# Kernel tuning notes

Hardware: AMD Instinct MI355X
Metric: run time of the kernel (lower is better)

## Reference

```python
import jax, jax.numpy as jnp
import numpy as np

N_NODES = 50000
N_EDGES = 800000
D_FEAT = 64
EDGE_DIM = 64


def setup_inputs() -> dict:
    key = jax.random.key(0)
    k1, k2, k3, k4 = jax.random.split(key, 4)
    node_feats = jax.random.normal(k1, (N_NODES, D_FEAT), dtype=jnp.float32)
    senders = jax.random.randint(k2, (N_EDGES,), 0, N_NODES, dtype=jnp.int32)
    receivers = jax.random.randint(k3, (N_EDGES,), 0, N_NODES, dtype=jnp.int32)
    # Dense(edge_dim) applied to concat([recv, send]) of width 2*D_FEAT
    W = jax.random.normal(k4, (2 * D_FEAT, EDGE_DIM), dtype=jnp.float32) / np.sqrt(2.0 * D_FEAT)
    b = jnp.zeros((EDGE_DIM,), dtype=jnp.float32)
    return {"node_feats": node_feats, "senders": senders, "receivers": receivers, "W": W, "b": b}


def reference(node_feats, senders, receivers, W, b):
    # gather node features at each edge endpoint: [E, D]
    feats_send = node_feats[senders]
    feats_recv = node_feats[receivers]
    # concat(recv, send) -> [E, 2D], Dense + tanh -> [E, edge_dim]
    edge_feats = jnp.concatenate([feats_recv, feats_send], axis=-1)
    return jnp.tanh(edge_feats @ W + b)
```

## Files before the change

kernel.cpp:

```cpp
#include <hip/hip_runtime.h>

#define N_EDGES 800000
#define N_NODES 50000
#define D 64

typedef __attribute__((ext_vector_type(8))) short bf16x8;
typedef __attribute__((ext_vector_type(4))) float f32x4;

#if __has_builtin(__builtin_amdgcn_exp2f)
#define EXP2F(x) __builtin_amdgcn_exp2f(x)
#else
#define EXP2F(x) __expf(0.69314718055994531f * (x))
#endif

__device__ __forceinline__ unsigned short f2bf(float f) {
    unsigned int u = __float_as_uint(f);
    u += 0x7fffu + ((u >> 16) & 1u);
    return (unsigned short)(u >> 16);
}
__device__ __forceinline__ unsigned int pack2(float a, float b) {
    return (unsigned int)f2bf(a) | ((unsigned int)f2bf(b) << 16);
}

__global__ __launch_bounds__(256) void prep(
    const float* __restrict__ nf, const float* __restrict__ W,
    unsigned short* __restrict__ nodes_bf, unsigned short* __restrict__ wfrag)
{
    if (blockIdx.x == gridDim.x - 1) {
#pragma unroll
        for (int i = 0; i < 4; ++i) {
            const int idx = i * 256 + threadIdx.x;
            const int ki = idx >> 8;
            const int nt = (idx >> 6) & 3;
            const int l  = idx & 63;
            const int m  = l & 15, q = l >> 4;
            const int kbase = ki * 32 + q * 8;
            const int n = nt * 16 + m;
            unsigned short* dst = wfrag + idx * 8;
#pragma unroll
            for (int j = 0; j < 8; ++j)
                dst[j] = f2bf(W[(kbase + j) * D + n]);
        }
    } else {
        const long base = ((long)blockIdx.x * 256 + threadIdx.x) * 8;
        if (base < (long)N_NODES * D) {
            const float4 lo = *(const float4*)(nf + base);
            const float4 hi = *(const float4*)(nf + base + 4);
            uint4 p;
            p.x = pack2(lo.x, lo.y);
            p.y = pack2(lo.z, lo.w);
            p.z = pack2(hi.x, hi.y);
            p.w = pack2(hi.z, hi.w);
            *(uint4*)(nodes_bf + base) = p;
        }
    }
}

__global__ __launch_bounds__(256) void edge_mlp(
    const unsigned short* __restrict__ nodes_bf,
    const bf16x8*        __restrict__ wfrag,
    const int*   __restrict__ senders,
    const int*   __restrict__ receivers,
    const float* __restrict__ bias,
    float*       __restrict__ out)
{
    __shared__ bf16x8 lds_b[1024];

#pragma unroll
    for (int i = 0; i < 4; ++i) {
        const int idx = i * 256 + threadIdx.x;
        lds_b[idx] = wfrag[idx];
    }
    __syncthreads();

    const int lane = threadIdx.x & 63;
    const int m    = lane & 15;
    const int q    = lane >> 4;
    const long wid = (long)blockIdx.x * 4 + (threadIdx.x >> 6);
    const long e0  = wid * 64;

    const int rv = receivers[e0 + lane];
    const int sv = senders[e0 + lane];
    int nidx[2][4];
#pragma unroll
    for (int mt = 0; mt < 4; ++mt) {
        nidx[0][mt] = __shfl(rv, mt * 16 + m, 64);
        nidx[1][mt] = __shfl(sv, mt * 16 + m, 64);
    }

    f32x4 acc[4][4];
#pragma unroll
    for (int mt = 0; mt < 4; ++mt)
#pragma unroll
        for (int nt = 0; nt < 4; ++nt)
            acc[mt][nt] = (f32x4)0.0f;

#pragma unroll
    for (int ki = 0; ki < 4; ++ki) {
        const int k0 = ki * 32 + q * 8;

        bf16x8 bfrag[4];
#pragma unroll
        for (int nt = 0; nt < 4; ++nt)
            bfrag[nt] = lds_b[(ki * 4 + nt) * 64 + lane];

        bf16x8 afrag[4];
#pragma unroll
        for (int mt = 0; mt < 4; ++mt) {
            const int node = nidx[ki >> 1][mt];
            afrag[mt] = *(const bf16x8*)(nodes_bf + node * D + (k0 & 63));
        }

#pragma unroll
        for (int mt = 0; mt < 4; ++mt)
#pragma unroll
            for (int nt = 0; nt < 4; ++nt)
                acc[mt][nt] = __builtin_amdgcn_mfma_f32_16x16x32_bf16(
                    bfrag[nt], afrag[mt], acc[mt][nt], 0, 0, 0);
    }

    const float C2L = 2.8853900817779268f;
    f32x4 cb[4];
#pragma unroll
    for (int nt = 0; nt < 4; ++nt) {
        const float4 b4 = *(const float4*)(bias + nt * 16 + q * 4);
        cb[nt] = (f32x4){b4.x * C2L, b4.y * C2L, b4.z * C2L, b4.w * C2L};
    }

#pragma unroll
    for (int mt = 0; mt < 4; ++mt) {
        float* op = out + (e0 + mt * 16 + m) * D + q * 4;
#pragma unroll
        for (int nt = 0; nt < 4; ++nt) {
            f32x4 y;
#pragma unroll
            for (int r = 0; r < 4; ++r) {
                const float t  = EXP2F(__builtin_fmaf(acc[mt][nt][r], C2L, cb[nt][r]));
                const float rc = __builtin_amdgcn_rcpf(t + 1.0f);
                y[r] = __builtin_fmaf(-2.0f, rc, 1.0f);
            }
            __builtin_nontemporal_store(y, (f32x4*)(op + nt * 16));
        }
    }
}

extern "C" void kernel_launch(void* const* d_in, const int* in_sizes, int n_in,
                              void* d_out, int out_size, void* d_ws, size_t ws_size,
                              hipStream_t stream) {
    const float* node_feats = (const float*)d_in[0];
    const int*   senders    = (const int*)d_in[1];
    const int*   receivers  = (const int*)d_in[2];
    const float* W          = (const float*)d_in[3];
    const float* bias       = (const float*)d_in[4];
    float*       out        = (float*)d_out;

    unsigned short* nodes_bf = (unsigned short*)d_ws;
    unsigned short* wfrag    = (unsigned short*)((char*)d_ws + (size_t)N_NODES * D * 2);

    const int node_blocks = ((N_NODES * D / 8) + 255) / 256;
    prep<<<node_blocks + 1, 256, 0, stream>>>(node_feats, W, nodes_bf, wfrag);

    const int n_blocks = N_EDGES / 256;
    edge_mlp<<<n_blocks, 256, 0, stream>>>(nodes_bf, (const bf16x8*)wfrag,
                                           senders, receivers, bias, out);
}
```

Measured before the change: 269.0 us.

## Project node features through W halves before gathering per edge

Uses linearity of the dense layer: each node's features are multiplied by the receiver and sender halves of W once per node (50k rows), storing two fp32 projection tables. The edge kernel then gathers two projected rows, adds them with bias and applies tanh, so the per-edge matmul is gone. The cost is that each gathered row is now fp32 (256 B) instead of bf16 (128 B), which doubles gather traffic, plus an extra kernel launch and a 25.6 MB intermediate write.

```diff
diff --git a/kernel.cpp b/kernel.cpp
--- a/kernel.cpp
+++ b/kernel.cpp
@@ -22,50 +22,30 @@
     return (unsigned int)f2bf(a) | ((unsigned int)f2bf(b) << 16);
 }
 
-__global__ __launch_bounds__(256) void prep(
-    const float* __restrict__ nf, const float* __restrict__ W,
-    unsigned short* __restrict__ nodes_bf, unsigned short* __restrict__ wfrag)
+__global__ __launch_bounds__(256) void prep_w(
+    const float* __restrict__ W, unsigned short* __restrict__ wfrag)
 {
-    if (blockIdx.x == gridDim.x - 1) {
 #pragma unroll
-        for (int i = 0; i < 4; ++i) {
-            const int idx = i * 256 + threadIdx.x;
-            const int ki = idx >> 8;
-            const int nt = (idx >> 6) & 3;
-            const int l  = idx & 63;
-            const int m  = l & 15, q = l >> 4;
-            const int kbase = ki * 32 + q * 8;
-            const int n = nt * 16 + m;
-            unsigned short* dst = wfrag + idx * 8;
+    for (int i = 0; i < 4; ++i) {
+        const int idx = i * 256 + threadIdx.x;
+        const int ki = idx >> 8;
+        const int nt = (idx >> 6) & 3;
+        const int l  = idx & 63;
+        const int m  = l & 15, q = l >> 4;
+        const int kbase = ki * 32 + q * 8;
+        const int n = nt * 16 + m;
+        unsigned short* dst = wfrag + idx * 8;
 #pragma unroll
-            for (int j = 0; j < 8; ++j)
-                dst[j] = f2bf(W[(kbase + j) * D + n]);
-        }
-    } else {
-        const long base = ((long)blockIdx.x * 256 + threadIdx.x) * 8;
-        if (base < (long)N_NODES * D) {
-            const float4 lo = *(const float4*)(nf + base);
-            const float4 hi = *(const float4*)(nf + base + 4);
-            uint4 p;
-            p.x = pack2(lo.x, lo.y);
-            p.y = pack2(lo.z, lo.w);
-            p.z = pack2(hi.x, hi.y);
-            p.w = pack2(hi.z, hi.w);
-            *(uint4*)(nodes_bf + base) = p;
-        }
+        for (int j = 0; j < 8; ++j)
+            dst[j] = f2bf(W[(kbase + j) * D + n]);
     }
 }
 
-__global__ __launch_bounds__(256) void edge_mlp(
-    const unsigned short* __restrict__ nodes_bf,
-    const bf16x8*        __restrict__ wfrag,
-    const int*   __restrict__ senders,
-    const int*   __restrict__ receivers,
-    const float* __restrict__ bias,
-    float*       __restrict__ out)
+__global__ __launch_bounds__(256) void node_proj(
+    const float* __restrict__ nf, const bf16x8* __restrict__ wfrag,
+    float* __restrict__ Pr, float* __restrict__ Ps)
 {
     __shared__ bf16x8 lds_b[1024];
-
 #pragma unroll
     for (int i = 0; i < 4; ++i) {
         const int idx = i * 256 + threadIdx.x;
@@ -76,71 +56,98 @@
     const int lane = threadIdx.x & 63;
     const int m    = lane & 15;
     const int q    = lane >> 4;
-    const long wid = (long)blockIdx.x * 4 + (threadIdx.x >> 6);
-    const long e0  = wid * 64;
+    const int wid  = blockIdx.x * 4 + (threadIdx.x >> 6);
+    const int n0   = wid * 64;
 
-    const int rv = receivers[e0 + lane];
-    const int sv = senders[e0 + lane];
-    int nidx[2][4];
+    bf16x8 a[2][4];
 #pragma unroll
     for (int mt = 0; mt < 4; ++mt) {
-        nidx[0][mt] = __shfl(rv, mt * 16 + m, 64);
-        nidx[1][mt] = __shfl(sv, mt * 16 + m, 64);
+        const int row = n0 + mt * 16 + m;
+        const int rl  = row < N_NODES ? row : N_NODES - 1;
+        const float* rp = nf + (long)rl * D;
+#pragma unroll
+        for (int kk = 0; kk < 2; ++kk) {
+            const float4 lo = *(const float4*)(rp + kk * 32 + q * 8);
+            const float4 hi = *(const float4*)(rp + kk * 32 + q * 8 + 4);
+            union { bf16x8 v; unsigned int u[4]; } cv;
+            cv.u[0] = pack2(lo.x, lo.y);
+            cv.u[1] = pack2(lo.z, lo.w);
+            cv.u[2] = pack2(hi.x, hi.y);
+            cv.u[3] = pack2(hi.z, hi.w);
+            a[kk][mt] = cv.v;
+        }
     }
 
-    f32x4 acc[4][4];
 #pragma unroll
-    for (int mt = 0; mt < 4; ++mt)
-#pragma unroll
-        for (int nt = 0; nt < 4; ++nt)
-            acc[mt][nt] = (f32x4)0.0f;
-
-#pragma unroll
-    for (int ki = 0; ki < 4; ++ki) {
-        const int k0 = ki * 32 + q * 8;
-
-        bf16x8 bfrag[4];
-#pragma unroll
-        for (int nt = 0; nt < 4; ++nt)
-            bfrag[nt] = lds_b[(ki * 4 + nt) * 64 + lane];
-
-        bf16x8 afrag[4];
-#pragma unroll
-        for (int mt = 0; mt < 4; ++mt) {
-            const int node = nidx[ki >> 1][mt];
-            afrag[mt] = *(const bf16x8*)(nodes_bf + node * D + (k0 & 63));
-        }
-
+    for (int tab = 0; tab < 2; ++tab) {
+        f32x4 acc[4][4];
 #pragma unroll
         for (int mt = 0; mt < 4; ++mt)
 #pragma unroll
             for (int nt = 0; nt < 4; ++nt)
-                acc[mt][nt] = __builtin_amdgcn_mfma_f32_16x16x32_bf16(
-                    bfrag[nt], afrag[mt], acc[mt][nt], 0, 0, 0);
+                acc[mt][nt] = (f32x4)0.0f;
+
+#pragma unroll
+        for (int ki2 = 0; ki2 < 2; ++ki2) {
+#pragma unroll
+            for (int nt = 0; nt < 4; ++nt) {
+                const bf16x8 bf = lds_b[((tab * 2 + ki2) * 4 + nt) * 64 + lane];
+#pragma unroll
+                for (int mt = 0; mt < 4; ++mt)
+                    acc[mt][nt] = __builtin_amdgcn_mfma_f32_16x16x32_bf16(
+                        bf, a[ki2][mt], acc[mt][nt], 0, 0, 0);
+            }
+        }
+
+        float* __restrict__ P = tab ? Ps : Pr;
+#pragma unroll
+        for (int mt = 0; mt < 4; ++mt) {
+            const int row = n0 + mt * 16 + m;
+            if (row < N_NODES) {
+                float* op = P + (long)row * D + q * 4;
+#pragma unroll
+                for (int nt = 0; nt < 4; ++nt)
+                    *(f32x4*)(op + nt * 16) = acc[mt][nt];
+            }
+        }
+    }
+}
+
+__global__ __launch_bounds__(256) void edge_act(
+    const float* __restrict__ Pr, const float* __restrict__ Ps,
+    const int*   __restrict__ senders, const int* __restrict__ receivers,
+    const float* __restrict__ bias, float* __restrict__ out)
+{
+    const int t = blockIdx.x * 256 + threadIdx.x;
+    const int e = t >> 2;
+    const int c = t & 3;
+
+    const int r = receivers[e];
+    const int s = senders[e];
+    const float* pr = Pr + (long)r * D + c * 4;
+    const float* ps = Ps + (long)s * D + c * 4;
+    float*       op = out + (long)e * D + c * 4;
+
+    f32x4 pa[4], pb[4], bb[4];
+#pragma unroll
+    for (int s4 = 0; s4 < 4; ++s4) {
+        pa[s4] = *(const f32x4*)(pr + s4 * 16);
+        pb[s4] = *(const f32x4*)(ps + s4 * 16);
+        bb[s4] = *(const f32x4*)(bias + s4 * 16 + c * 4);
     }
 
     const float C2L = 2.8853900817779268f;
-    f32x4 cb[4];
 #pragma unroll
-    for (int nt = 0; nt < 4; ++nt) {
-        const float4 b4 = *(const float4*)(bias + nt * 16 + q * 4);
-        cb[nt] = (f32x4){b4.x * C2L, b4.y * C2L, b4.z * C2L, b4.w * C2L};
-    }
-
+    for (int s4 = 0; s4 < 4; ++s4) {
+        const f32x4 x = pa[s4] + pb[s4];
+        f32x4 y;
 #pragma unroll
-    for (int mt = 0; mt < 4; ++mt) {
-        float* op = out + (e0 + mt * 16 + m) * D + q * 4;
-#pragma unroll
-        for (int nt = 0; nt < 4; ++nt) {
-            f32x4 y;
-#pragma unroll
-            for (int r = 0; r < 4; ++r) {
-                const float t  = EXP2F(__builtin_fmaf(acc[mt][nt][r], C2L, cb[nt][r]));
-                const float rc = __builtin_amdgcn_rcpf(t + 1.0f);
-                y[r] = __builtin_fmaf(-2.0f, rc, 1.0f);
-            }
-            __builtin_nontemporal_store(y, (f32x4*)(op + nt * 16));
+        for (int k = 0; k < 4; ++k) {
+            const float tt = EXP2F(__builtin_fmaf(x[k], C2L, bb[s4][k] * C2L));
+            const float rc = __builtin_amdgcn_rcpf(tt + 1.0f);
+            y[k] = __builtin_fmaf(-2.0f, rc, 1.0f);
         }
+        __builtin_nontemporal_store(y, (f32x4*)(op + s4 * 16));
     }
 }
 
@@ -154,13 +161,15 @@
     const float* bias       = (const float*)d_in[4];
     float*       out        = (float*)d_out;
 
-    unsigned short* nodes_bf = (unsigned short*)d_ws;
-    unsigned short* wfrag    = (unsigned short*)((char*)d_ws + (size_t)N_NODES * D * 2);
+    float* Pr = (float*)d_ws;
+    float* Ps = Pr + (size_t)N_NODES * D;
+    unsigned short* wfrag = (unsigned short*)(Ps + (size_t)N_NODES * D);
 
-    const int node_blocks = ((N_NODES * D / 8) + 255) / 256;
-    prep<<<node_blocks + 1, 256, 0, stream>>>(node_feats, W, nodes_bf, wfrag);
+    prep_w<<<1, 256, 0, stream>>>(W, wfrag);
 
-    const int n_blocks = N_EDGES / 256;
-    edge_mlp<<<n_blocks, 256, 0, stream>>>(nodes_bf, (const bf16x8*)wfrag,
-                                           senders, receivers, bias, out);
+    const int np_blocks = (N_NODES + 255) / 256;
+    node_proj<<<np_blocks, 256, 0, stream>>>(node_feats, (const bf16x8*)wfrag, Pr, Ps);
+
+    const int ea_blocks = (N_EDGES * 4) / 256;
+    edge_act<<<ea_blocks, 256, 0, stream>>>(Pr, Ps, senders, receivers, bias, out);
 }
```

After: 277.9 us. +3.3%, slower.
